# Kernel optimization log

Measured on AMD Instinct MI355X. Metric: run time of the kernel, lower is better.

## Reference

```python
import jax, jax.numpy as jnp
import numpy as np

SEQ, BATCH = 512, 128
FEAT_CH, EMBED = 1024, 1024
N_LANG = 8  # tgt_lang_toks = [0..7]


def setup_inputs() -> dict:
    key = jax.random.key(0)
    k_feat, k_tok, k_w, k_b = jax.random.split(key, 4)
    feat = jax.random.normal(k_feat, (SEQ, BATCH, FEAT_CH), dtype=jnp.float32)
    tgt_lang_toks = jax.random.randint(k_tok, (BATCH,), 0, N_LANG, dtype=jnp.int64)
    # stacked per-language Linear params: W[l] is [embed, feat] (torch Linear layout), b[l] is [embed]
    bound = 1.0 / np.sqrt(FEAT_CH)
    W = jax.random.uniform(k_w, (N_LANG, EMBED, FEAT_CH), minval=-bound, maxval=bound, dtype=jnp.float32)
    b = jax.random.uniform(k_b, (N_LANG, EMBED), minval=-bound, maxval=bound, dtype=jnp.float32)
    return {"feat": feat, "W": W, "b": b, "tgt_lang_toks": tgt_lang_toks}


def reference(feat, W, b, tgt_lang_toks):
    # Each batch column uses the Linear of its language token. Since the
    # language token values equal their index in tgt_lang_toks=[0..7], the
    # per-group mask/gather/scatter of the original collapses to a per-batch
    # weight gather + batched matmul (grouped GEMM as dense dispatch).
    toks = tgt_lang_toks.astype(jnp.int32)
    W_sel = W[toks]          # [B, E, F]
    b_sel = b[toks]          # [B, E]
    # [S,B,F] x [B,E,F] -> [S,B,E]
    out = jnp.einsum('sbf,bef->sbe', feat, W_sel) + b_sel[None, :, :]
    return out
```

## Files before the change

### kernel.cpp

```cpp
#include <hip/hip_runtime.h>
#include <hip/hip_bf16.h>

#define SEQ   512
#define BATCH 128
#define FEAT  1024
#define EMBED 1024
#define NLANG 8

typedef __attribute__((ext_vector_type(8))) short bf16x8;
typedef __attribute__((ext_vector_type(4))) float f32x4;
typedef unsigned short ushort_t;

__device__ __forceinline__ unsigned pk2(float a, float b) {
  float2 f; f.x = a; f.y = b;
  __hip_bfloat162 h = __float22bfloat162_rn(f);
  union { __hip_bfloat162 h2; unsigned u; } cv;
  cv.h2 = h;
  return cv.u;
}

__device__ __forceinline__ bf16x8 cvt8(float4 lo, float4 hi) {
  union { bf16x8 v; unsigned u[4]; } q;
  q.u[0] = pk2(lo.x, lo.y); q.u[1] = pk2(lo.z, lo.w);
  q.u[2] = pk2(hi.x, hi.y); q.u[3] = pk2(hi.z, hi.w);
  return q.v;
}

__device__ __forceinline__ void gld16(const void* g, void* l) {
  __builtin_amdgcn_global_load_lds(
      (const __attribute__((address_space(1))) void*)g,
      (__attribute__((address_space(3))) void*)l, 16, 0, 0);
}

__global__ __launch_bounds__(256) void convert_w_kernel(
    const float* __restrict__ Wf, ushort_t* __restrict__ Wbf)
{
  const int n = (NLANG * EMBED * FEAT) / 4;
  for (int c = blockIdx.x * 256 + threadIdx.x; c < n; c += gridDim.x * 256) {
    float4 v = ((const float4*)Wf)[c];
    uint2 o; o.x = pk2(v.x, v.y); o.y = pk2(v.z, v.w);
    *(uint2*)(Wbf + ((size_t)c << 2)) = o;
  }
}

__global__ __launch_bounds__(512, 2) void grouped_gemm_fused(
    const float* __restrict__ feat,
    const ushort_t* __restrict__ Wbf,
    const float* __restrict__ bias,
    const int*   __restrict__ toks,
    float*       __restrict__ out)
{
  extern __shared__ char ldsraw[];
  ushort_t* Af = (ushort_t*)ldsraw;
  ushort_t* Bf = (ushort_t*)(ldsraw + 32768);
  __shared__ int tokarr[128];
  __shared__ unsigned long long ballots[2][8];
  __shared__ int perm[128];
  __shared__ int rowsrc[256];

  const int tid = threadIdx.x;
  const int l   = tid & 63;
  const int w   = tid >> 6;
  const int wr  = w >> 2;
  const int wc  = w & 3;

  const int bid = blockIdx.x;
  const int L   = (bid & 7) * 128 + (bid >> 3);
  const int et  = L & 3;
  const int mt  = (L >> 7) * 32 + ((L >> 2) & 31);
  const int m0  = mt * 256;
  const int e0  = et * 256;

  if (tid < 128) tokarr[tid] = toks[tid];
  __syncthreads();
  if (tid < 128) {
    int myt = tokarr[tid];
#pragma unroll
    for (int lg = 0; lg < 8; ++lg) {
      unsigned long long bl = __ballot(myt == lg);
      if (l == 0) ballots[w][lg] = bl;
    }
  }
  __syncthreads();

  int lsel = 0, base = 0, csel = 1, boff_sel = 0;
  {
    int cum = 0, boff = 0;
#pragma unroll
    for (int lg = 0; lg < 8; ++lg) {
      int c = __popcll(ballots[0][lg]) + __popcll(ballots[1][lg]);
      int seg = c << 9;
      bool in = (m0 >= cum) && (m0 < cum + seg);
      if (in) { lsel = lg; base = cum; csel = c; boff_sel = boff; }
      cum += seg; boff += c;
    }
  }

  if (tid < 128) {
    int myt = tokarr[tid];
    unsigned long long ltm = (1ull << l) - 1ull;
    int rank = (w == 0) ? __popcll(ballots[0][myt] & ltm)
                        : __popcll(ballots[0][myt]) + __popcll(ballots[1][myt] & ltm);
    int boff2 = 0;
#pragma unroll
    for (int lg = 0; lg < 8; ++lg) {
      int c = __popcll(ballots[0][lg]) + __popcll(ballots[1][lg]);
      boff2 += (lg < myt) ? c : 0;
    }
    perm[boff2 + rank] = tid;
  }
  __syncthreads();
  if (tid < 256) {
    int local = m0 - base + tid;
    int s = local / csel;
    int j = local - s * csel;
    rowsrc[tid] = s * BATCH + perm[boff_sel + j];
  }
  __syncthreads();

  const int arow = tid >> 1;
  const int ah   = tid & 1;
  const float* aSrcP = feat + (size_t)rowsrc[arow] * FEAT + ah * 16;
  const int sAw     = (arow >> 1) & 3;
  const int wchunk0 = arow * 4 + ((2 * ah) ^ sAw);
  const int wchunk1 = arow * 4 + ((2 * ah + 1) ^ sAw);
  float4 ar0, ar1, ar2, ar3;

  const int ca  = w * 128 + l;
  const int rwB = ca >> 2;
  const int ccB = ca & 3;
  const int sB  = (rwB >> 1) & 3;
  const ushort_t* bS0 = Wbf + ((size_t)lsel * EMBED + e0 + rwB) * FEAT + ((ccB ^ sB) * 8);
  const ushort_t* bS1 = bS0 + (size_t)16 * FEAT;
  const int bD0 = (w * 128) * 8;
  const int bD1 = (w * 128 + 64) * 8;

  const int kc  = l >> 4;
  const int rA  = wr * 128 + (l & 15);
  const int aRd = rA * 32 + ((kc ^ ((rA >> 1) & 3)) * 8);
  const int rB  = wc * 64 + (l & 15);
  const int bRd = rB * 32 + ((kc ^ ((rB >> 1) & 3)) * 8);

  f32x4 acc[8][4] = {};

#define LOAD_A(kt)                                                         \
  do { const float* _p = aSrcP + (kt) * 32;                                \
    ar0 = *(const float4*)(_p);      ar1 = *(const float4*)(_p + 4);       \
    ar2 = *(const float4*)(_p + 8);  ar3 = *(const float4*)(_p + 12); } while (0)
#define WRITE_A(buf)                                                       \
  do { bf16x8* _wp = (bf16x8*)(Af + (buf) * 8192);                         \
    _wp[wchunk0] = cvt8(ar0, ar1);                                         \
    _wp[wchunk1] = cvt8(ar2, ar3); } while (0)
#define STAGE_B(kt, buf)                                                   \
  do { const int _o = (kt) * 32;                                           \
    gld16(bS0 + _o, Bf + (buf) * 8192 + bD0);                              \
    gld16(bS1 + _o, Bf + (buf) * 8192 + bD1); } while (0)

#define GRAN(G, J, DOCVT, DOSTAGE, ENDWAIT, ENDBAR)                        \
  do {                                                                     \
    if (DOCVT) { WRITE_A(((J) + 1) & 1); }                                 \
    if (DOSTAGE) { LOAD_A((G) + 2); STAGE_B((G) + 2, ((J) + 2) % 3); }     \
    __builtin_amdgcn_sched_barrier(0);                                     \
    const ushort_t* Ar_ = Af + ((J) & 1) * 8192;                           \
    const ushort_t* Br_ = Bf + ((J) % 3) * 8192;                           \
    bf16x8 af[8], bfq[4];                                                  \
    _Pragma("unroll") for (int mf = 0; mf < 8; ++mf)                       \
        af[mf] = *(const bf16x8*)(Ar_ + aRd + mf * 512);                   \
    _Pragma("unroll") for (int nf = 0; nf < 4; ++nf)                       \
        bfq[nf] = *(const bf16x8*)(Br_ + bRd + nf * 512);                  \
    asm volatile("s_waitcnt lgkmcnt(0)" ::: "memory");                     \
    __builtin_amdgcn_sched_barrier(0);                                     \
    __builtin_amdgcn_s_setprio(1);                                         \
    _Pragma("unroll") for (int mf = 0; mf < 8; ++mf)                       \
        _Pragma("unroll") for (int nf = 0; nf < 4; ++nf)                   \
            acc[mf][nf] = __builtin_amdgcn_mfma_f32_16x16x32_bf16(         \
                af[mf], bfq[nf], acc[mf][nf], 0, 0, 0);                    \
    __builtin_amdgcn_s_setprio(0);                                         \
    asm volatile(ENDWAIT ::: "memory");                                    \
    if (ENDBAR) { __builtin_amdgcn_s_barrier();                            \
                  __builtin_amdgcn_sched_barrier(0); }                     \
  } while (0)

  LOAD_A(0);
  STAGE_B(0, 0);
  WRITE_A(0);
  LOAD_A(1);
  STAGE_B(1, 1);
  __builtin_amdgcn_sched_barrier(0);
  asm volatile("s_waitcnt lgkmcnt(0)" ::: "memory");
  asm volatile("s_waitcnt vmcnt(6)" ::: "memory");
  __builtin_amdgcn_s_barrier();
  __builtin_amdgcn_sched_barrier(0);

#pragma unroll 1
  for (int gb = 0; gb < 30; gb += 6) {
    GRAN(gb + 0, 0, true, true, "s_waitcnt vmcnt(6)", true);
    GRAN(gb + 1, 1, true, true, "s_waitcnt vmcnt(6)", true);
    GRAN(gb + 2, 2, true, true, "s_waitcnt vmcnt(6)", true);
    GRAN(gb + 3, 3, true, true, "s_waitcnt vmcnt(6)", true);
    GRAN(gb + 4, 4, true, true, "s_waitcnt vmcnt(6)", true);
    GRAN(gb + 5, 5, true, true, "s_waitcnt vmcnt(6)", true);
  }
  GRAN(30, 0, true, false, "s_waitcnt vmcnt(0)", true);
  GRAN(31, 1, false, false, "s_nop 0", false);

#undef GRAN
#undef LOAD_A
#undef WRITE_A
#undef STAGE_B

  const int col = l & 15;
  const int r4  = (l >> 4) * 4;
  float bvv[4];
#pragma unroll
  for (int nf = 0; nf < 4; ++nf)
    bvv[nf] = bias[lsel * EMBED + e0 + wc * 64 + nf * 16 + col];
#pragma unroll
  for (int mf = 0; mf < 8; ++mf) {
#pragma unroll
    for (int j = 0; j < 4; ++j) {
      const size_t ro = (size_t)rowsrc[wr * 128 + mf * 16 + r4 + j] * EMBED;
#pragma unroll
      for (int nf = 0; nf < 4; ++nf)
        out[ro + e0 + wc * 64 + nf * 16 + col] = acc[mf][nf][j] + bvv[nf];
    }
  }
}

__global__ __launch_bounds__(256, 2) void grouped_proj_fused(
    const float* __restrict__ feat, const float* __restrict__ Wt,
    const float* __restrict__ bias, const int* __restrict__ toks,
    float* __restrict__ out)
{
  __shared__ uint4 As[1024];
  __shared__ uint4 Bs[1024];
  __shared__ int tokarr[128];
  __shared__ unsigned long long ballots[2][8];
  __shared__ int perm[128];
  __shared__ int rowsrc[128];

  const int tid  = threadIdx.x;
  const int lane = tid & 63;
  const int wv   = tid >> 6;
  const int wr   = wv >> 1;
  const int wc   = wv & 1;
  const int bid = blockIdx.x;
  const int xcd = bid & 7;
  const int sq  = bid >> 3;
  const int et  = sq & 7;
  const int mt  = (sq >> 3) * 8 + xcd;
  const int m0  = mt * 128;
  const int e0  = et * 128;

  if (tid < 128) tokarr[tid] = toks[tid];
  __syncthreads();
  if (tid < 128) {
    int myt = tokarr[tid];
#pragma unroll
    for (int lg = 0; lg < 8; ++lg) {
      unsigned long long bl = __ballot(myt == lg);
      if (lane == 0) ballots[wv][lg] = bl;
    }
  }
  __syncthreads();
  int lsel = 0, base = 0, csel = 1, boff_sel = 0;
  {
    int cum = 0, boff = 0;
#pragma unroll
    for (int lg = 0; lg < 8; ++lg) {
      int c = __popcll(ballots[0][lg]) + __popcll(ballots[1][lg]);
      int seg = c << 9;
      bool in = (m0 >= cum) && (m0 < cum + seg);
      if (in) { lsel = lg; base = cum; csel = c; boff_sel = boff; }
      cum += seg; boff += c;
    }
  }
  if (tid < 128) {
    int myt = tokarr[tid];
    unsigned long long ltm = (1ull << lane) - 1ull;
    int rank = (wv == 0) ? __popcll(ballots[0][myt] & ltm)
                         : __popcll(ballots[0][myt]) + __popcll(ballots[1][myt] & ltm);
    int boff2 = 0;
#pragma unroll
    for (int lg = 0; lg < 8; ++lg) {
      int c = __popcll(ballots[0][lg]) + __popcll(ballots[1][lg]);
      boff2 += (lg < myt) ? c : 0;
    }
    perm[boff2 + rank] = tid;
  }
  __syncthreads();
  if (tid < 128) {
    int local = m0 - base + tid;
    int s = local / csel;
    int j = local - s * csel;
    rowsrc[tid] = s * BATCH + perm[boff_sel + j];
  }
  __syncthreads();

  int slot_i[4];
  const float* aptr[4];
  const float* bptr[4];
#pragma unroll
  for (int it = 0; it < 4; ++it) {
    int c    = it * 256 + tid;
    int kg   = c & 7;
    int row  = c >> 3;
    int ksub = kg & 3;
    int kk   = kg >> 2;
    int frag = row >> 4;
    slot_i[it] = (kk * 8 + frag) * 64 + ((row & 15) ^ (ksub << 1) ^ kk) + ksub * 16;
    aptr[it] = feat + (size_t)rowsrc[row] * FEAT + kg * 8;
    bptr[it] = Wt + ((size_t)lsel * EMBED + e0 + row) * FEAT + kg * 8;
  }

  f32x4 acc[4][4] = {};
  for (int k0 = 0; k0 < FEAT; k0 += 64) {
    __syncthreads();
#pragma unroll
    for (int it = 0; it < 4; ++it) {
      float4 alo = *(const float4*)(aptr[it] + k0);
      float4 ahi = *(const float4*)(aptr[it] + k0 + 4);
      uint4 av;
      av.x = pk2(alo.x, alo.y); av.y = pk2(alo.z, alo.w);
      av.z = pk2(ahi.x, ahi.y); av.w = pk2(ahi.z, ahi.w);
      As[slot_i[it]] = av;
      float4 blo = *(const float4*)(bptr[it] + k0);
      float4 bhi = *(const float4*)(bptr[it] + k0 + 4);
      uint4 bv;
      bv.x = pk2(blo.x, blo.y); bv.y = pk2(blo.z, blo.w);
      bv.z = pk2(bhi.x, bhi.y); bv.w = pk2(bhi.z, bhi.w);
      Bs[slot_i[it]] = bv;
    }
    __syncthreads();
#pragma unroll
    for (int kk = 0; kk < 2; ++kk) {
      const int ksr = lane >> 4;
      const int sw  = ((lane & 15) ^ (ksr << 1) ^ kk) + ksr * 16;
      bf16x8 af[4], bfr[4];
#pragma unroll
      for (int mi = 0; mi < 4; ++mi)
        af[mi] = ((const bf16x8*)As)[(kk * 8 + wr * 4 + mi) * 64 + sw];
#pragma unroll
      for (int ni = 0; ni < 4; ++ni)
        bfr[ni] = ((const bf16x8*)Bs)[(kk * 8 + wc * 4 + ni) * 64 + sw];
#pragma unroll
      for (int mi = 0; mi < 4; ++mi)
#pragma unroll
        for (int ni = 0; ni < 4; ++ni)
          acc[mi][ni] = __builtin_amdgcn_mfma_f32_16x16x32_bf16(
              af[mi], bfr[ni], acc[mi][ni], 0, 0, 0);
    }
  }

  const int col = lane & 15;
  const int r0  = (lane >> 4) * 4;
  float bvv[4];
#pragma unroll
  for (int ni = 0; ni < 4; ++ni)
    bvv[ni] = bias[lsel * EMBED + e0 + wc * 64 + ni * 16 + col];
#pragma unroll
  for (int mi = 0; mi < 4; ++mi) {
#pragma unroll
    for (int j = 0; j < 4; ++j) {
      const size_t ro = (size_t)rowsrc[wr * 64 + mi * 16 + r0 + j] * EMBED;
#pragma unroll
      for (int ni = 0; ni < 4; ++ni)
        out[ro + e0 + wc * 64 + ni * 16 + col] = acc[mi][ni][j] + bvv[ni];
    }
  }
}

extern "C" void kernel_launch(void* const* d_in, const int* in_sizes, int n_in,
                              void* d_out, int out_size, void* d_ws, size_t ws_size,
                              hipStream_t stream) {
  const float* feat = (const float*)d_in[0];
  const float* W    = (const float*)d_in[1];
  const float* bias = (const float*)d_in[2];
  const int*   toks = (const int*)d_in[3];
  float* out = (float*)d_out;

  const size_t wbf_bytes = (size_t)NLANG * EMBED * FEAT * 2;

  if (ws_size >= wbf_bytes) {
    ushort_t* Wbf = (ushort_t*)d_ws;
    convert_w_kernel<<<512, 256, 0, stream>>>(W, Wbf);
    (void)hipFuncSetAttribute((const void*)grouped_gemm_fused,
                              hipFuncAttributeMaxDynamicSharedMemorySize, 81920);
    const int nblk = (SEQ * BATCH / 256) * (EMBED / 256);
    grouped_gemm_fused<<<nblk, 512, 81920, stream>>>(feat, Wbf, bias, toks, out);
  } else {
    grouped_proj_fused<<<(SEQ * BATCH / 128) * (EMBED / 128), 256, 0, stream>>>(
        feat, W, bias, toks, out);
  }
}
```

Baseline: 300.5 us.

## Double-buffer A staging registers and defer fp32-to-bf16 LDS write past MFMAs

```diff
diff --git a/kernel.cpp b/kernel.cpp
--- a/kernel.cpp
+++ b/kernel.cpp
@@ -124,7 +124,8 @@
   const int sAw     = (arow >> 1) & 3;
   const int wchunk0 = arow * 4 + ((2 * ah) ^ sAw);
   const int wchunk1 = arow * 4 + ((2 * ah + 1) ^ sAw);
-  float4 ar0, ar1, ar2, ar3;
+  float4 arA0, arA1, arA2, arA3;
+  float4 arB0, arB1, arB2, arB3;
 
   const int ca  = w * 128 + l;
   const int rwB = ca >> 2;
@@ -143,14 +144,24 @@
 
   f32x4 acc[8][4] = {};
 
-#define LOAD_A(kt)                                                         \
+#define LOAD_A(kt, SET)                                                    \
   do { const float* _p = aSrcP + (kt) * 32;                                \
-    ar0 = *(const float4*)(_p);      ar1 = *(const float4*)(_p + 4);       \
-    ar2 = *(const float4*)(_p + 8);  ar3 = *(const float4*)(_p + 12); } while (0)
-#define WRITE_A(buf)                                                       \
+    if ((SET) == 0) {                                                      \
+      arA0 = *(const float4*)(_p);      arA1 = *(const float4*)(_p + 4);   \
+      arA2 = *(const float4*)(_p + 8);  arA3 = *(const float4*)(_p + 12);  \
+    } else {                                                               \
+      arB0 = *(const float4*)(_p);      arB1 = *(const float4*)(_p + 4);   \
+      arB2 = *(const float4*)(_p + 8);  arB3 = *(const float4*)(_p + 12);  \
+    } } while (0)
+#define WRITE_A(buf, SET)                                                  \
   do { bf16x8* _wp = (bf16x8*)(Af + (buf) * 8192);                         \
-    _wp[wchunk0] = cvt8(ar0, ar1);                                         \
-    _wp[wchunk1] = cvt8(ar2, ar3); } while (0)
+    if ((SET) == 0) {                                                      \
+      _wp[wchunk0] = cvt8(arA0, arA1);                                     \
+      _wp[wchunk1] = cvt8(arA2, arA3);                                     \
+    } else {                                                               \
+      _wp[wchunk0] = cvt8(arB0, arB1);                                     \
+      _wp[wchunk1] = cvt8(arB2, arB3);                                     \
+    } } while (0)
 #define STAGE_B(kt, buf)                                                   \
   do { const int _o = (kt) * 32;                                           \
     gld16(bS0 + _o, Bf + (buf) * 8192 + bD0);                              \
@@ -158,9 +169,7 @@
 
 #define GRAN(G, J, DOCVT, DOSTAGE, ENDWAIT, ENDBAR)                        \
   do {                                                                     \
-    if (DOCVT) { WRITE_A(((J) + 1) & 1); }                                 \
-    if (DOSTAGE) { LOAD_A((G) + 2); STAGE_B((G) + 2, ((J) + 2) % 3); }     \
-    __builtin_amdgcn_sched_barrier(0);                                     \
+    if (DOSTAGE) { LOAD_A((G) + 2, (J) & 1); STAGE_B((G) + 2, ((J) + 2) % 3); } \
     const ushort_t* Ar_ = Af + ((J) & 1) * 8192;                           \
     const ushort_t* Br_ = Bf + ((J) % 3) * 8192;                           \
     bf16x8 af[8], bfq[4];                                                  \
@@ -176,32 +185,32 @@
             acc[mf][nf] = __builtin_amdgcn_mfma_f32_16x16x32_bf16(         \
                 af[mf], bfq[nf], acc[mf][nf], 0, 0, 0);                    \
     __builtin_amdgcn_s_setprio(0);                                         \
+    if (DOCVT) { WRITE_A(((J) + 1) & 1, ((J) + 1) & 1); }                  \
     asm volatile(ENDWAIT ::: "memory");                                    \
     if (ENDBAR) { __builtin_amdgcn_s_barrier();                            \
                   __builtin_amdgcn_sched_barrier(0); }                     \
   } while (0)
 
-  LOAD_A(0);
+  LOAD_A(0, 0);
   STAGE_B(0, 0);
-  WRITE_A(0);
-  LOAD_A(1);
+  LOAD_A(1, 1);
   STAGE_B(1, 1);
+  WRITE_A(0, 0);
   __builtin_amdgcn_sched_barrier(0);
-  asm volatile("s_waitcnt lgkmcnt(0)" ::: "memory");
-  asm volatile("s_waitcnt vmcnt(6)" ::: "memory");
+  asm volatile("s_waitcnt vmcnt(6) lgkmcnt(0)" ::: "memory");
   __builtin_amdgcn_s_barrier();
   __builtin_amdgcn_sched_barrier(0);
 
 #pragma unroll 1
   for (int gb = 0; gb < 30; gb += 6) {
-    GRAN(gb + 0, 0, true, true, "s_waitcnt vmcnt(6)", true);
-    GRAN(gb + 1, 1, true, true, "s_waitcnt vmcnt(6)", true);
-    GRAN(gb + 2, 2, true, true, "s_waitcnt vmcnt(6)", true);
-    GRAN(gb + 3, 3, true, true, "s_waitcnt vmcnt(6)", true);
-    GRAN(gb + 4, 4, true, true, "s_waitcnt vmcnt(6)", true);
-    GRAN(gb + 5, 5, true, true, "s_waitcnt vmcnt(6)", true);
-  }
-  GRAN(30, 0, true, false, "s_waitcnt vmcnt(0)", true);
+    GRAN(gb + 0, 0, true, true, "s_waitcnt vmcnt(6) lgkmcnt(0)", true);
+    GRAN(gb + 1, 1, true, true, "s_waitcnt vmcnt(6) lgkmcnt(0)", true);
+    GRAN(gb + 2, 2, true, true, "s_waitcnt vmcnt(6) lgkmcnt(0)", true);
+    GRAN(gb + 3, 3, true, true, "s_waitcnt vmcnt(6) lgkmcnt(0)", true);
+    GRAN(gb + 4, 4, true, true, "s_waitcnt vmcnt(6) lgkmcnt(0)", true);
+    GRAN(gb + 5, 5, true, true, "s_waitcnt vmcnt(6) lgkmcnt(0)", true);
+  }
+  GRAN(30, 0, true, false, "s_waitcnt vmcnt(0) lgkmcnt(0)", true);
   GRAN(31, 1, false, false, "s_nop 0", false);
 
 #undef GRAN
```

After: 305.7 us. No clear change (+1.7%).

## Shrink GEMM M-tile to 128 with triple-buffered A and higher occupancy

Applied to the files above, without the earlier changes.

```diff
diff --git a/kernel.cpp b/kernel.cpp
--- a/kernel.cpp
+++ b/kernel.cpp
@@ -43,7 +43,7 @@
   }
 }
 
-__global__ __launch_bounds__(512, 2) void grouped_gemm_fused(
+__global__ __launch_bounds__(512, 4) void grouped_gemm_fused(
     const float* __restrict__ feat,
     const ushort_t* __restrict__ Wbf,
     const float* __restrict__ bias,
@@ -51,12 +51,12 @@
     float*       __restrict__ out)
 {
   extern __shared__ char ldsraw[];
-  ushort_t* Af = (ushort_t*)ldsraw;
-  ushort_t* Bf = (ushort_t*)(ldsraw + 32768);
+  ushort_t* Alds = (ushort_t*)ldsraw;
+  ushort_t* Blds = (ushort_t*)(ldsraw + 24576);
   __shared__ int tokarr[128];
   __shared__ unsigned long long ballots[2][8];
   __shared__ int perm[128];
-  __shared__ int rowsrc[256];
+  __shared__ int rowsrc[128];
 
   const int tid = threadIdx.x;
   const int l   = tid & 63;
@@ -65,10 +65,10 @@
   const int wc  = w & 3;
 
   const int bid = blockIdx.x;
-  const int L   = (bid & 7) * 128 + (bid >> 3);
+  const int L   = (bid & 7) * 256 + (bid >> 3);
   const int et  = L & 3;
-  const int mt  = (L >> 7) * 32 + ((L >> 2) & 31);
-  const int m0  = mt * 256;
+  const int mt  = L >> 2;
+  const int m0  = mt * 128;
   const int e0  = et * 256;
 
   if (tid < 128) tokarr[tid] = toks[tid];
@@ -110,7 +110,7 @@
     perm[boff2 + rank] = tid;
   }
   __syncthreads();
-  if (tid < 256) {
+  if (tid < 128) {
     int local = m0 - base + tid;
     int s = local / csel;
     int j = local - s * csel;
@@ -118,17 +118,16 @@
   }
   __syncthreads();
 
-  const int arow = tid >> 1;
-  const int ah   = tid & 1;
-  const float* aSrcP = feat + (size_t)rowsrc[arow] * FEAT + ah * 16;
-  const int sAw     = (arow >> 1) & 3;
-  const int wchunk0 = arow * 4 + ((2 * ah) ^ sAw);
-  const int wchunk1 = arow * 4 + ((2 * ah + 1) ^ sAw);
-  float4 ar0, ar1, ar2, ar3;
-
-  const int ca  = w * 128 + l;
-  const int rwB = ca >> 2;
-  const int ccB = ca & 3;
+  const int arow = tid >> 2;
+  const int aq   = tid & 2 ? (tid & 3) : (tid & 3);
+  const float* aSrcP = feat + (size_t)rowsrc[arow] * FEAT + (tid & 3) * 8;
+  const int wchunk = arow * 4 + ((tid & 3) ^ ((arow >> 1) & 3));
+  float4 ar0, ar1;
+  (void)aq;
+
+  const int ch  = w * 128 + l;
+  const int rwB = ch >> 2;
+  const int ccB = ch & 3;
   const int sB  = (rwB >> 1) & 3;
   const ushort_t* bS0 = Wbf + ((size_t)lsel * EMBED + e0 + rwB) * FEAT + ((ccB ^ sB) * 8);
   const ushort_t* bS1 = bS0 + (size_t)16 * FEAT;
@@ -136,42 +135,36 @@
   const int bD1 = (w * 128 + 64) * 8;
 
   const int kc  = l >> 4;
-  const int rA  = wr * 128 + (l & 15);
+  const int rA  = wr * 64 + (l & 15);
   const int aRd = rA * 32 + ((kc ^ ((rA >> 1) & 3)) * 8);
   const int rB  = wc * 64 + (l & 15);
   const int bRd = rB * 32 + ((kc ^ ((rB >> 1) & 3)) * 8);
 
-  f32x4 acc[8][4] = {};
+  f32x4 acc[4][4] = {};
 
 #define LOAD_A(kt)                                                         \
   do { const float* _p = aSrcP + (kt) * 32;                                \
-    ar0 = *(const float4*)(_p);      ar1 = *(const float4*)(_p + 4);       \
-    ar2 = *(const float4*)(_p + 8);  ar3 = *(const float4*)(_p + 12); } while (0)
+    ar0 = *(const float4*)(_p); ar1 = *(const float4*)(_p + 4); } while (0)
 #define WRITE_A(buf)                                                       \
-  do { bf16x8* _wp = (bf16x8*)(Af + (buf) * 8192);                         \
-    _wp[wchunk0] = cvt8(ar0, ar1);                                         \
-    _wp[wchunk1] = cvt8(ar2, ar3); } while (0)
+  do { ((bf16x8*)(Alds + (buf) * 4096))[wchunk] = cvt8(ar0, ar1); } while (0)
 #define STAGE_B(kt, buf)                                                   \
   do { const int _o = (kt) * 32;                                           \
-    gld16(bS0 + _o, Bf + (buf) * 8192 + bD0);                              \
-    gld16(bS1 + _o, Bf + (buf) * 8192 + bD1); } while (0)
-
-#define GRAN(G, J, DOCVT, DOSTAGE, ENDWAIT, ENDBAR)                        \
+    gld16(bS0 + _o, Blds + (buf) * 8192 + bD0);                            \
+    gld16(bS1 + _o, Blds + (buf) * 8192 + bD1); } while (0)
+
+#define BODY(t, J, DOWRITE, DOLOAD, ENDWAIT, ENDBAR)                       \
   do {                                                                     \
-    if (DOCVT) { WRITE_A(((J) + 1) & 1); }                                 \
-    if (DOSTAGE) { LOAD_A((G) + 2); STAGE_B((G) + 2, ((J) + 2) % 3); }     \
-    __builtin_amdgcn_sched_barrier(0);                                     \
-    const ushort_t* Ar_ = Af + ((J) & 1) * 8192;                           \
-    const ushort_t* Br_ = Bf + ((J) % 3) * 8192;                           \
-    bf16x8 af[8], bfq[4];                                                  \
-    _Pragma("unroll") for (int mf = 0; mf < 8; ++mf)                       \
+    if (DOWRITE) { WRITE_A(((J) + 1) % 3); }                               \
+    if (DOLOAD)  { LOAD_A((t) + 2); STAGE_B((t) + 2, ((J) + 2) % 3); }     \
+    const ushort_t* Ar_ = Alds + (J) * 4096;                               \
+    const ushort_t* Br_ = Blds + (J) * 8192;                               \
+    bf16x8 af[4], bfq[4];                                                  \
+    _Pragma("unroll") for (int mf = 0; mf < 4; ++mf)                       \
         af[mf] = *(const bf16x8*)(Ar_ + aRd + mf * 512);                   \
     _Pragma("unroll") for (int nf = 0; nf < 4; ++nf)                       \
         bfq[nf] = *(const bf16x8*)(Br_ + bRd + nf * 512);                  \
-    asm volatile("s_waitcnt lgkmcnt(0)" ::: "memory");                     \
-    __builtin_amdgcn_sched_barrier(0);                                     \
     __builtin_amdgcn_s_setprio(1);                                         \
-    _Pragma("unroll") for (int mf = 0; mf < 8; ++mf)                       \
+    _Pragma("unroll") for (int mf = 0; mf < 4; ++mf)                       \
         _Pragma("unroll") for (int nf = 0; nf < 4; ++nf)                   \
             acc[mf][nf] = __builtin_amdgcn_mfma_f32_16x16x32_bf16(         \
                 af[mf], bfq[nf], acc[mf][nf], 0, 0, 0);                    \
@@ -182,29 +175,25 @@
   } while (0)
 
   LOAD_A(0);
+  WRITE_A(0);
   STAGE_B(0, 0);
-  WRITE_A(0);
+  STAGE_B(1, 1);
   LOAD_A(1);
-  STAGE_B(1, 1);
-  __builtin_amdgcn_sched_barrier(0);
-  asm volatile("s_waitcnt lgkmcnt(0)" ::: "memory");
-  asm volatile("s_waitcnt vmcnt(6)" ::: "memory");
+  asm volatile("s_waitcnt vmcnt(4) lgkmcnt(0)" ::: "memory");
   __builtin_amdgcn_s_barrier();
   __builtin_amdgcn_sched_barrier(0);
 
 #pragma unroll 1
-  for (int gb = 0; gb < 30; gb += 6) {
-    GRAN(gb + 0, 0, true, true, "s_waitcnt vmcnt(6)", true);
-    GRAN(gb + 1, 1, true, true, "s_waitcnt vmcnt(6)", true);
-    GRAN(gb + 2, 2, true, true, "s_waitcnt vmcnt(6)", true);
-    GRAN(gb + 3, 3, true, true, "s_waitcnt vmcnt(6)", true);
-    GRAN(gb + 4, 4, true, true, "s_waitcnt vmcnt(6)", true);
-    GRAN(gb + 5, 5, true, true, "s_waitcnt vmcnt(6)", true);
-  }
-  GRAN(30, 0, true, false, "s_waitcnt vmcnt(0)", true);
-  GRAN(31, 1, false, false, "s_nop 0", false);
-
-#undef GRAN
+  for (int gg = 0; gg < 10; ++gg) {
+    const int g = gg * 3;
+    BODY(g + 0, 0, true, true, "s_waitcnt vmcnt(4) lgkmcnt(0)", true);
+    BODY(g + 1, 1, true, true, "s_waitcnt vmcnt(4) lgkmcnt(0)", true);
+    BODY(g + 2, 2, true, true, "s_waitcnt vmcnt(4) lgkmcnt(0)", true);
+  }
+  BODY(30, 0, true, false, "s_waitcnt vmcnt(0) lgkmcnt(0)", true);
+  BODY(31, 1, false, false, "s_nop 0", false);
+
+#undef BODY
 #undef LOAD_A
 #undef WRITE_A
 #undef STAGE_B
@@ -216,10 +205,10 @@
   for (int nf = 0; nf < 4; ++nf)
     bvv[nf] = bias[lsel * EMBED + e0 + wc * 64 + nf * 16 + col];
 #pragma unroll
-  for (int mf = 0; mf < 8; ++mf) {
+  for (int mf = 0; mf < 4; ++mf) {
 #pragma unroll
     for (int j = 0; j < 4; ++j) {
-      const size_t ro = (size_t)rowsrc[wr * 128 + mf * 16 + r4 + j] * EMBED;
+      const size_t ro = (size_t)rowsrc[wr * 64 + mf * 16 + r4 + j] * EMBED;
 #pragma unroll
       for (int nf = 0; nf < 4; ++nf)
         out[ro + e0 + wc * 64 + nf * 16 + col] = acc[mf][nf][j] + bvv[nf];
@@ -385,9 +374,9 @@
     ushort_t* Wbf = (ushort_t*)d_ws;
     convert_w_kernel<<<512, 256, 0, stream>>>(W, Wbf);
     (void)hipFuncSetAttribute((const void*)grouped_gemm_fused,
-                              hipFuncAttributeMaxDynamicSharedMemorySize, 81920);
-    const int nblk = (SEQ * BATCH / 256) * (EMBED / 256);
-    grouped_gemm_fused<<<nblk, 512, 81920, stream>>>(feat, Wbf, bias, toks, out);
+                              hipFuncAttributeMaxDynamicSharedMemorySize, 73728);
+    const int nblk = (SEQ * BATCH / 128) * (EMBED / 256);
+    grouped_gemm_fused<<<nblk, 512, 73728, stream>>>(feat, Wbf, bias, toks, out);
   } else {
     grouped_proj_fused<<<(SEQ * BATCH / 128) * (EMBED / 128), 256, 0, stream>>>(
         feat, W, bias, toks, out);
```

Measured after the change: 257.3 us. -14.4%, faster.

## Stage fp32 A tiles into LDS via async loads, convert to bf16 in-LDS

Applied to the files above, without the earlier changes.

```diff
diff --git a/kernel.cpp b/kernel.cpp
--- a/kernel.cpp
+++ b/kernel.cpp
@@ -19,10 +19,10 @@
   return cv.u;
 }
 
-__device__ __forceinline__ bf16x8 cvt8(float4 lo, float4 hi) {
+__device__ __forceinline__ bf16x8 cvt8(f32x4 lo, f32x4 hi) {
   union { bf16x8 v; unsigned u[4]; } q;
-  q.u[0] = pk2(lo.x, lo.y); q.u[1] = pk2(lo.z, lo.w);
-  q.u[2] = pk2(hi.x, hi.y); q.u[3] = pk2(hi.z, hi.w);
+  q.u[0] = pk2(lo[0], lo[1]); q.u[1] = pk2(lo[2], lo[3]);
+  q.u[2] = pk2(hi[0], hi[1]); q.u[3] = pk2(hi[2], hi[3]);
   return q.v;
 }
 
@@ -43,16 +43,14 @@
   }
 }
 
-__global__ __launch_bounds__(512, 2) void grouped_gemm_fused(
+__global__ __launch_bounds__(512, 2) void grouped_gemm_cvt1(
     const float* __restrict__ feat,
     const ushort_t* __restrict__ Wbf,
     const float* __restrict__ bias,
     const int*   __restrict__ toks,
     float*       __restrict__ out)
 {
-  extern __shared__ char ldsraw[];
-  ushort_t* Af = (ushort_t*)ldsraw;
-  ushort_t* Bf = (ushort_t*)(ldsraw + 32768);
+  extern __shared__ ushort_t lds[];
   __shared__ int tokarr[128];
   __shared__ unsigned long long ballots[2][8];
   __shared__ int perm[128];
@@ -118,13 +116,20 @@
   }
   __syncthreads();
 
-  const int arow = tid >> 1;
-  const int ah   = tid & 1;
-  const float* aSrcP = feat + (size_t)rowsrc[arow] * FEAT + ah * 16;
-  const int sAw     = (arow >> 1) & 3;
-  const int wchunk0 = arow * 4 + ((2 * ah) ^ sAw);
-  const int wchunk1 = arow * 4 + ((2 * ah + 1) ^ sAw);
-  float4 ar0, ar1, ar2, ar3;
+  const float* aS[4];
+#pragma unroll
+  for (int i = 0; i < 4; ++i) {
+    const int row = w * 32 + i * 8 + (l >> 3);
+    aS[i] = feat + (size_t)rowsrc[row] * FEAT + (l & 7) * 4;
+  }
+  const int aD[4] = { (w * 4 + 0) * 512, (w * 4 + 1) * 512,
+                      (w * 4 + 2) * 512, (w * 4 + 3) * 512 };
+
+  const int cr  = tid >> 1;
+  const int chh = tid & 1;
+  const int csw = (cr >> 1) & 3;
+  const int wc0 = cr * 4 + ((2 * chh) ^ csw);
+  const int wc1 = cr * 4 + ((2 * chh + 1) ^ csw);
 
   const int ca  = w * 128 + l;
   const int rwB = ca >> 2;
@@ -143,26 +148,35 @@
 
   f32x4 acc[8][4] = {};
 
-#define LOAD_A(kt)                                                         \
-  do { const float* _p = aSrcP + (kt) * 32;                                \
-    ar0 = *(const float4*)(_p);      ar1 = *(const float4*)(_p + 4);       \
-    ar2 = *(const float4*)(_p + 8);  ar3 = *(const float4*)(_p + 12); } while (0)
-#define WRITE_A(buf)                                                       \
-  do { bf16x8* _wp = (bf16x8*)(Af + (buf) * 8192);                         \
-    _wp[wchunk0] = cvt8(ar0, ar1);                                         \
-    _wp[wchunk1] = cvt8(ar2, ar3); } while (0)
-#define STAGE_B(kt, buf)                                                   \
+#define STAGE_A(kt, abuf)                                                  \
   do { const int _o = (kt) * 32;                                           \
-    gld16(bS0 + _o, Bf + (buf) * 8192 + bD0);                              \
-    gld16(bS1 + _o, Bf + (buf) * 8192 + bD1); } while (0)
-
-#define GRAN(G, J, DOCVT, DOSTAGE, ENDWAIT, ENDBAR)                        \
+    gld16(aS[0] + _o, lds + (abuf) * 16384 + aD[0]);                       \
+    gld16(aS[1] + _o, lds + (abuf) * 16384 + aD[1]);                       \
+    gld16(aS[2] + _o, lds + (abuf) * 16384 + aD[2]);                       \
+    gld16(aS[3] + _o, lds + (abuf) * 16384 + aD[3]); } while (0)
+#define STAGE_B(kt, bbuf)                                                  \
+  do { const int _o = (kt) * 32;                                           \
+    gld16(bS0 + _o, lds + 40960 + (bbuf) * 8192 + bD0);                    \
+    gld16(bS1 + _o, lds + 40960 + (bbuf) * 8192 + bD1); } while (0)
+#define CONV(abuf)                                                         \
   do {                                                                     \
-    if (DOCVT) { WRITE_A(((J) + 1) & 1); }                                 \
-    if (DOSTAGE) { LOAD_A((G) + 2); STAGE_B((G) + 2, ((J) + 2) % 3); }     \
+    const f32x4* _fp = (const f32x4*)(lds + (abuf) * 16384);               \
+    f32x4 q0 = _fp[4 * tid + 0], q1 = _fp[4 * tid + 1];                    \
+    f32x4 q2 = _fp[4 * tid + 2], q3 = _fp[4 * tid + 3];                    \
+    bf16x8* _bp = (bf16x8*)(lds + 32768);                                  \
+    _bp[wc0] = cvt8(q0, q1);                                               \
+    _bp[wc1] = cvt8(q2, q3);                                               \
+  } while (0)
+
+#define BODY(g, AJ, BJ, DOSTAGE, ENDWAIT, ENDBAR)                          \
+  do {                                                                     \
+    CONV(AJ);                                                              \
+    asm volatile("s_waitcnt lgkmcnt(0)" ::: "memory");                     \
+    __builtin_amdgcn_s_barrier();                     \
     __builtin_amdgcn_sched_barrier(0);                                     \
-    const ushort_t* Ar_ = Af + ((J) & 1) * 8192;                           \
-    const ushort_t* Br_ = Bf + ((J) % 3) * 8192;                           \
+    if (DOSTAGE) { STAGE_A((g) + 2, AJ); STAGE_B((g) + 2, ((BJ) + 2) % 3); } \
+    const ushort_t* Ar_ = lds + 32768;                                     \
+    const ushort_t* Br_ = lds + 40960 + (BJ) * 8192;                       \
     bf16x8 af[8], bfq[4];                                                  \
     _Pragma("unroll") for (int mf = 0; mf < 8; ++mf)                       \
         af[mf] = *(const bf16x8*)(Ar_ + aRd + mf * 512);                   \
@@ -181,32 +195,27 @@
                   __builtin_amdgcn_sched_barrier(0); }                     \
   } while (0)
 
-  LOAD_A(0);
-  STAGE_B(0, 0);
-  WRITE_A(0);
-  LOAD_A(1);
-  STAGE_B(1, 1);
-  __builtin_amdgcn_sched_barrier(0);
-  asm volatile("s_waitcnt lgkmcnt(0)" ::: "memory");
+  STAGE_A(0, 0); STAGE_B(0, 0);
+  STAGE_A(1, 1); STAGE_B(1, 1);
   asm volatile("s_waitcnt vmcnt(6)" ::: "memory");
   __builtin_amdgcn_s_barrier();
   __builtin_amdgcn_sched_barrier(0);
 
 #pragma unroll 1
   for (int gb = 0; gb < 30; gb += 6) {
-    GRAN(gb + 0, 0, true, true, "s_waitcnt vmcnt(6)", true);
-    GRAN(gb + 1, 1, true, true, "s_waitcnt vmcnt(6)", true);
-    GRAN(gb + 2, 2, true, true, "s_waitcnt vmcnt(6)", true);
-    GRAN(gb + 3, 3, true, true, "s_waitcnt vmcnt(6)", true);
-    GRAN(gb + 4, 4, true, true, "s_waitcnt vmcnt(6)", true);
-    GRAN(gb + 5, 5, true, true, "s_waitcnt vmcnt(6)", true);
-  }
-  GRAN(30, 0, true, false, "s_waitcnt vmcnt(0)", true);
-  GRAN(31, 1, false, false, "s_nop 0", false);
-
-#undef GRAN
-#undef LOAD_A
-#undef WRITE_A
+    BODY(gb + 0, 0, 0, true, "s_waitcnt vmcnt(6)", true);
+    BODY(gb + 1, 1, 1, true, "s_waitcnt vmcnt(6)", true);
+    BODY(gb + 2, 0, 2, true, "s_waitcnt vmcnt(6)", true);
+    BODY(gb + 3, 1, 0, true, "s_waitcnt vmcnt(6)", true);
+    BODY(gb + 4, 0, 1, true, "s_waitcnt vmcnt(6)", true);
+    BODY(gb + 5, 1, 2, true, "s_waitcnt vmcnt(6)", true);
+  }
+  BODY(30, 0, 0, false, "s_waitcnt vmcnt(0)", true);
+  BODY(31, 1, 1, false, "s_nop 0", false);
+
+#undef BODY
+#undef CONV
+#undef STAGE_A
 #undef STAGE_B
 
   const int col = l & 15;
@@ -384,10 +393,10 @@
   if (ws_size >= wbf_bytes) {
     ushort_t* Wbf = (ushort_t*)d_ws;
     convert_w_kernel<<<512, 256, 0, stream>>>(W, Wbf);
-    (void)hipFuncSetAttribute((const void*)grouped_gemm_fused,
-                              hipFuncAttributeMaxDynamicSharedMemorySize, 81920);
+    (void)hipFuncSetAttribute((const void*)grouped_gemm_cvt1,
+                              hipFuncAttributeMaxDynamicSharedMemorySize, 131072);
     const int nblk = (SEQ * BATCH / 256) * (EMBED / 256);
-    grouped_gemm_fused<<<nblk, 512, 81920, stream>>>(feat, Wbf, bias, toks, out);
+    grouped_gemm_cvt1<<<nblk, 512, 131072, stream>>>(feat, Wbf, bias, toks, out);
   } else {
     grouped_proj_fused<<<(SEQ * BATCH / 128) * (EMBED / 128), 256, 0, stream>>>(
         feat, W, bias, toks, out);
```

Measured after the change: 248.1 us. 1.21x faster.
